# Kernel optimization log

Measured on AMD Instinct MI355X. Metric: run time of the kernel, lower is better.

The kernel has to match this reference:

```python
import jax, jax.numpy as jnp
import numpy as np

N = 10000      # nodes
F_IN = 256     # input feature dim
H1 = 128       # hidden_dim1
H2 = 64        # hidden_dim2 (latent)
E = 320000     # edges (avg degree 32)


def setup_inputs() -> dict:
    key = jax.random.key(0)
    ks = jax.random.split(key, 10)
    x = jax.random.normal(ks[0], (N, F_IN), dtype=jnp.float32)
    edge_index = jax.random.randint(ks[1], (2, E), 0, N, dtype=jnp.int64)
    edge_weight = jax.random.uniform(ks[2], (E,), dtype=jnp.float32)
    s1 = 1.0 / np.sqrt(F_IN)
    s2 = 1.0 / np.sqrt(H1)
    W1 = jax.random.normal(ks[3], (F_IN, H1), dtype=jnp.float32) * s1
    b1 = jnp.zeros((H1,), dtype=jnp.float32)
    W2 = jax.random.normal(ks[4], (H1, H2), dtype=jnp.float32) * s2
    b2 = jnp.zeros((H2,), dtype=jnp.float32)
    W3 = jax.random.normal(ks[5], (H1, H2), dtype=jnp.float32) * s2
    b3 = jnp.zeros((H2,), dtype=jnp.float32)
    return {"x": x, "edge_index": edge_index, "edge_weight": edge_weight,
            "W1": W1, "b1": b1, "W2": W2, "b2": b2, "W3": W3, "b3": b3}


def _gcn_norm(edge_index, edge_weight, n):
    # add self-loops with weight 1, symmetric deg^-1/2 normalization (PyG GCNConv)
    loop = jnp.arange(n)
    row = jnp.concatenate([edge_index[0], loop])
    col = jnp.concatenate([edge_index[1], loop])
    w = jnp.concatenate([edge_weight, jnp.ones((n,), edge_weight.dtype)])
    deg = jax.ops.segment_sum(w, col, num_segments=n)
    dis = jnp.where(deg > 0, jax.lax.rsqrt(deg), 0.0)
    norm = dis[row] * w * dis[col]
    return row, col, norm


def _gcn_conv(h, W, b, row, col, norm, n):
    hw = h @ W                                   # [N, out] transform first (PyG order)
    out = jax.ops.segment_sum(norm[:, None] * hw[row], col, num_segments=n)
    return out + b


def reference(x, edge_index, edge_weight, W1, b1, W2, b2, W3, b3):
    n = x.shape[0]
    row, col, norm = _gcn_norm(edge_index, edge_weight, n)
    h1 = jax.nn.relu(_gcn_conv(x, W1, b1, row, col, norm, n))
    mu = _gcn_conv(h1, W2, b2, row, col, norm, n)
    logvar = _gcn_conv(h1, W3, b3, row, col, norm, n)
    # eval mode: reparameterize -> mu, dropout inactive, decoder act = identity
    z = mu
    adj = z @ z.T                                # [N, N] inner-product decode
    return adj, mu, logvar
```

## Files before the change

### kernel.cpp

```cpp
#include <hip/hip_runtime.h>

#define N_NODES 10000
#define F_IN    256
#define H1      128
#define H2      64
#define NEDGE   320000
#define M_TOT   (NEDGE + N_NODES)

typedef __attribute__((ext_vector_type(8))) short          s16v8;
typedef __attribute__((ext_vector_type(8))) unsigned short u16v8;
typedef __attribute__((ext_vector_type(4))) float          f32v4;


__global__ void k_init(float* deg, int* cnt) {
    int i = blockIdx.x * blockDim.x + threadIdx.x;
    if (i < N_NODES) { deg[i] = 1.0f; cnt[i] = 1; }
}

__global__ void k_count(const int* __restrict__ ei, const float* __restrict__ w,
                        float* deg, int* cnt) {
    int e = blockIdx.x * blockDim.x + threadIdx.x;
    if (e < NEDGE) {
        int c = ei[NEDGE + e];
        atomicAdd(&deg[c], w[e]);
        atomicAdd(&cnt[c], 1);
    }
}

__global__ void k_scan(const int* __restrict__ cnt, int* __restrict__ ptr,
                       int* __restrict__ cur) {
    __shared__ int part[1024];
    int t = threadIdx.x;
    int base = t * 10;
    int local[10];
    int s = 0;
#pragma unroll
    for (int j = 0; j < 10; j++) {
        int idx = base + j;
        int v = (idx < N_NODES) ? cnt[idx] : 0;
        local[j] = s;
        s += v;
    }
    part[t] = s;
    __syncthreads();
    for (int off = 1; off < 1024; off <<= 1) {
        int v = (t >= off) ? part[t - off] : 0;
        __syncthreads();
        part[t] += v;
        __syncthreads();
    }
    int excl = t ? part[t - 1] : 0;
#pragma unroll
    for (int j = 0; j < 10; j++) {
        int idx = base + j;
        if (idx < N_NODES) {
            int p = excl + local[j];
            ptr[idx] = p;
            cur[idx] = p;
        }
    }
    if (t == 1023) ptr[N_NODES] = part[1023];
}

__global__ void k_scatter(const int* __restrict__ ei, const float* __restrict__ w,
                          const float* __restrict__ deg, int* cur,
                          int* __restrict__ src, float* __restrict__ wgt) {
    int t = blockIdx.x * blockDim.x + threadIdx.x;
    if (t >= M_TOT) return;
    int r, c; float nw;
    if (t < NEDGE) {
        r = ei[t];
        c = ei[NEDGE + t];
        nw = rsqrtf(deg[r]) * w[t] * rsqrtf(deg[c]);
    } else {
        r = c = t - NEDGE;
        float d = rsqrtf(deg[r]);
        nw = d * d;
    }
    int pos = atomicAdd(&cur[c], 1);
    src[pos] = r;
    wgt[pos] = nw;
}


__global__ __launch_bounds__(128) void k_gemm1(const float* __restrict__ x,
                                               const float* __restrict__ W1,
                                               float* __restrict__ hw) {
    __shared__ float xs[8 * F_IN];
    int i0 = blockIdx.x * 8;
    int t = threadIdx.x;
    const float4* xsrc = (const float4*)(x + (size_t)i0 * F_IN);
    float4* xd = (float4*)xs;
#pragma unroll
    for (int j = 0; j < 4; j++) xd[t + j * 128] = xsrc[t + j * 128];
    __syncthreads();
    float acc[8] = {0, 0, 0, 0, 0, 0, 0, 0};
    for (int k = 0; k < F_IN; k += 4) {
        float w0 = W1[(k + 0) * H1 + t];
        float w1 = W1[(k + 1) * H1 + t];
        float w2 = W1[(k + 2) * H1 + t];
        float w3 = W1[(k + 3) * H1 + t];
#pragma unroll
        for (int r = 0; r < 8; r++) {
            float4 xv = *(const float4*)&xs[r * F_IN + k];
            acc[r] += xv.x * w0 + xv.y * w1 + xv.z * w2 + xv.w * w3;
        }
    }
#pragma unroll
    for (int r = 0; r < 8; r++) hw[(size_t)(i0 + r) * H1 + t] = acc[r];
}

__global__ __launch_bounds__(128) void k_gemm23(const float* __restrict__ h1,
                                                const float* __restrict__ W2,
                                                const float* __restrict__ W3,
                                                float* __restrict__ t2,
                                                float* __restrict__ t3) {
    __shared__ float hs[8 * H1];
    int i0 = blockIdx.x * 8;
    int t = threadIdx.x;
    const float4* hsrc = (const float4*)(h1 + (size_t)i0 * H1);
    float4* hd = (float4*)hs;
#pragma unroll
    for (int j = 0; j < 2; j++) hd[t + j * 128] = hsrc[t + j * 128];
    __syncthreads();
    int f = t & 63;
    int sel = t >> 6;
    const float* W = sel ? W3 : W2;
    float acc[8] = {0, 0, 0, 0, 0, 0, 0, 0};
    for (int k = 0; k < H1; k += 4) {
        float w0 = W[(k + 0) * H2 + f];
        float w1 = W[(k + 1) * H2 + f];
        float w2 = W[(k + 2) * H2 + f];
        float w3 = W[(k + 3) * H2 + f];
#pragma unroll
        for (int r = 0; r < 8; r++) {
            float4 hv = *(const float4*)&hs[r * H1 + k];
            acc[r] += hv.x * w0 + hv.y * w1 + hv.z * w2 + hv.w * w3;
        }
    }
    float* o = sel ? t3 : t2;
#pragma unroll
    for (int r = 0; r < 8; r++) o[(size_t)(i0 + r) * H2 + f] = acc[r];
}


__global__ __launch_bounds__(128) void k_agg1(const int* __restrict__ ptr,
                                              const int* __restrict__ src,
                                              const float* __restrict__ wgt,
                                              const float* __restrict__ hw,
                                              const float* __restrict__ b1,
                                              float* __restrict__ h1) {
    int i = blockIdx.x;
    int f = threadIdx.x;
    int jb = ptr[i], je = ptr[i + 1];
    float acc = b1[f];
    for (int j = jb; j < je; j++)
        acc += wgt[j] * hw[(size_t)src[j] * H1 + f];
    h1[(size_t)i * H1 + f] = fmaxf(acc, 0.0f);
}

__global__ __launch_bounds__(128) void k_agg2(const int* __restrict__ ptr,
                                              const int* __restrict__ src,
                                              const float* __restrict__ wgt,
                                              const float* __restrict__ t2,
                                              const float* __restrict__ t3,
                                              const float* __restrict__ b2,
                                              const float* __restrict__ b3,
                                              float* __restrict__ mu,
                                              float* __restrict__ lv) {
    int i = blockIdx.x;
    int t = threadIdx.x;
    int f = t & 63;
    int sel = t >> 6;
    const float* tin = sel ? t3 : t2;
    float acc = sel ? b3[f] : b2[f];
    int jb = ptr[i], je = ptr[i + 1];
    for (int j = jb; j < je; j++)
        acc += wgt[j] * tin[(size_t)src[j] * H2 + f];
    float* o = sel ? lv : mu;
    o[(size_t)i * H2 + f] = acc;
}

__global__ __launch_bounds__(256, 1) void k_adj(const float* __restrict__ z,
                                                float* __restrict__ adj) {
    if (blockIdx.x < blockIdx.y) return;
    __shared__ __align__(16) unsigned short PAs[128 * 64];
    __shared__ __align__(16) unsigned short PBs[128 * 64];
    __shared__ __align__(16) unsigned short PLs[128 * 64];
    int tid = threadIdx.x;
    int rowBase = blockIdx.y * 128, colBase = blockIdx.x * 128;
    bool diag = (blockIdx.x == blockIdx.y);

    int lane = tid & 63;
    int wv   = tid >> 6;
    int wr = (wv >> 1) * 64;
    int wc = (wv & 1) * 64;
    int lrow = lane & 15;
    int lk   = lane >> 4;

    int sr   = tid & 127;
    int isB  = tid >> 7;
    int gbase = (isB ? colBase : rowBase) + sr;
    bool ok = gbase < N_NODES;
    const float* srcp = z + (size_t)gbase * 64;
    unsigned short* PH = isB ? PBs : PAs;
    int lslotBase = isB ? 4 : 0;
    int rb7 = sr & 7;

    auto stage = [&](int s) {
#pragma unroll
        for (int g = 0; g < 4; g++) {
            float v[8];
            if (ok) {
                float4 a = *(const float4*)(srcp + s * 32 + g * 8);
                float4 b = *(const float4*)(srcp + s * 32 + g * 8 + 4);
                v[0] = a.x; v[1] = a.y; v[2] = a.z; v[3] = a.w;
                v[4] = b.x; v[5] = b.y; v[6] = b.z; v[7] = b.w;
            } else {
#pragma unroll
                for (int q = 0; q < 8; q++) v[q] = 0.0f;
            }
            u16v8 hv, mv, lv8;
#pragma unroll
            for (int q = 0; q < 8; q++) {
                float xv = v[q];
                unsigned hu = __float_as_uint(xv) & 0xffff0000u;
                float r1 = xv - __uint_as_float(hu);
                unsigned mu2 = __float_as_uint(r1) & 0xffff0000u;
                float r2 = r1 - __uint_as_float(mu2);
                unsigned lu = __float_as_uint(r2) & 0xffff0000u;
                hv[q]  = (unsigned short)(hu >> 16);
                mv[q]  = (unsigned short)(mu2 >> 16);
                lv8[q] = (unsigned short)(lu >> 16);
            }
            int base = sr * 64;
            *reinterpret_cast<u16v8*>(PH  + base + (( g            ^ rb7) * 8)) = hv;
            *reinterpret_cast<u16v8*>(PH  + base + (((4 + g)       ^ rb7) * 8)) = mv;
            *reinterpret_cast<u16v8*>(PLs + base + (((lslotBase+g) ^ rb7) * 8)) = lv8;
        }
    };

    f32v4 acc[4][4];
#pragma unroll
    for (int i = 0; i < 4; i++)
#pragma unroll
        for (int j = 0; j < 4; j++) acc[i][j] = (f32v4)0.0f;

    s16v8 a0[4], a1[4], a2[4], b0[4], b1[4], b2[4];

#define LOADFRAGS()                                                        \
    {                                                                      \
        _Pragma("unroll")                                                  \
        for (int fq = 0; fq < 4; fq++) {                                   \
            int ra = wr + fq * 16 + lrow;                                  \
            int r7 = ra & 7;                                               \
            int ia = ra * 64;                                              \
            a0[fq] = *reinterpret_cast<const s16v8*>(&PAs[ia + ((lk       ^ r7) * 8)]); \
            a1[fq] = *reinterpret_cast<const s16v8*>(&PAs[ia + (((4 + lk) ^ r7) * 8)]); \
            a2[fq] = *reinterpret_cast<const s16v8*>(&PLs[ia + ((lk       ^ r7) * 8)]); \
            int rb = wc + fq * 16 + lrow;                                  \
            int q7 = rb & 7;                                               \
            int ib = rb * 64;                                              \
            b0[fq] = *reinterpret_cast<const s16v8*>(&PBs[ib + ((lk       ^ q7) * 8)]); \
            b1[fq] = *reinterpret_cast<const s16v8*>(&PBs[ib + (((4 + lk) ^ q7) * 8)]); \
            b2[fq] = *reinterpret_cast<const s16v8*>(&PLs[ib + (((4 + lk) ^ q7) * 8)]); \
        }                                                                  \
    }

#define MFMAS()                                                            \
    {                                                                      \
        _Pragma("unroll")                                                  \
        for (int i = 0; i < 4; i++) {                                      \
            _Pragma("unroll")                                              \
            for (int j = 0; j < 4; j++) {                                  \
                f32v4 c = acc[i][j];                                       \
                c = __builtin_amdgcn_mfma_f32_16x16x32_bf16(a0[i], b0[j], c, 0, 0, 0); \
                c = __builtin_amdgcn_mfma_f32_16x16x32_bf16(a0[i], b1[j], c, 0, 0, 0); \
                c = __builtin_amdgcn_mfma_f32_16x16x32_bf16(a1[i], b0[j], c, 0, 0, 0); \
                c = __builtin_amdgcn_mfma_f32_16x16x32_bf16(a0[i], b2[j], c, 0, 0, 0); \
                c = __builtin_amdgcn_mfma_f32_16x16x32_bf16(a2[i], b0[j], c, 0, 0, 0); \
                c = __builtin_amdgcn_mfma_f32_16x16x32_bf16(a1[i], b1[j], c, 0, 0, 0); \
                acc[i][j] = c;                                             \
            }                                                              \
        }                                                                  \
    }

    stage(0);
    __syncthreads();
    LOADFRAGS();
    __syncthreads();
    stage(1);
    MFMAS();
    __syncthreads();
    LOADFRAGS();
    MFMAS();

#undef LOADFRAGS
#undef MFMAS

#pragma unroll
    for (int i = 0; i < 4; i++) {
        int r0 = rowBase + wr + i * 16 + lk * 4;
#pragma unroll
        for (int j = 0; j < 4; j++) {
            int cg = colBase + wc + j * 16 + lrow;
            if (cg < N_NODES) {
#pragma unroll
                for (int v = 0; v < 4; v++) {
                    int rg = r0 + v;
                    if (rg < N_NODES)
                        adj[(size_t)rg * N_NODES + cg] = acc[i][j][v];
                }
                if (!diag)
                    *(float4*)&adj[(size_t)cg * N_NODES + r0] =
                        make_float4(acc[i][j][0], acc[i][j][1], acc[i][j][2], acc[i][j][3]);
            }
        }
    }
}


extern "C" void kernel_launch(void* const* d_in, const int* in_sizes, int n_in,
                              void* d_out, int out_size, void* d_ws, size_t ws_size,
                              hipStream_t stream) {
    const float* x  = (const float*)d_in[0];
    const int*   ei = (const int*)d_in[1];
    const float* w  = (const float*)d_in[2];
    const float* W1 = (const float*)d_in[3];
    const float* b1 = (const float*)d_in[4];
    const float* W2 = (const float*)d_in[5];
    const float* b2 = (const float*)d_in[6];
    const float* W3 = (const float*)d_in[7];
    const float* b3 = (const float*)d_in[8];

    float* out = (float*)d_out;
    float* adj = out;
    float* mu  = out + (size_t)N_NODES * N_NODES;
    float* lv  = mu + (size_t)N_NODES * H2;

    float* ws  = out + 80000000;
    float* deg = ws;
    int*   cnt = (int*)(ws + 10240);
    int*   ptr = (int*)(ws + 20480);
    int*   cur = (int*)(ws + 30720);
    int*   src = (int*)(ws + 40960);
    float* wgt = ws + 371200;
    float* hw  = ws + 701440;
    float* h1  = ws + 1981440;
    float* t2  = ws + 3261440;
    float* t3  = ws + 3901440;

    hipLaunchKernelGGL(k_init,    dim3((N_NODES + 255) / 256), dim3(256), 0, stream, deg, cnt);
    hipLaunchKernelGGL(k_count,   dim3((NEDGE + 255) / 256),   dim3(256), 0, stream, ei, w, deg, cnt);
    hipLaunchKernelGGL(k_scan,    dim3(1), dim3(1024), 0, stream, cnt, ptr, cur);
    hipLaunchKernelGGL(k_scatter, dim3((M_TOT + 255) / 256),   dim3(256), 0, stream, ei, w, deg, cur, src, wgt);
    hipLaunchKernelGGL(k_gemm1,   dim3(N_NODES / 8),  dim3(128), 0, stream, x, W1, hw);
    hipLaunchKernelGGL(k_agg1,    dim3(N_NODES),      dim3(128), 0, stream, ptr, src, wgt, hw, b1, h1);
    hipLaunchKernelGGL(k_gemm23,  dim3(N_NODES / 8),  dim3(128), 0, stream, h1, W2, W3, t2, t3);
    hipLaunchKernelGGL(k_agg2,    dim3(N_NODES),      dim3(128), 0, stream, ptr, src, wgt, t2, t3, b2, b3, mu, lv);

    dim3 g((N_NODES + 127) / 128, (N_NODES + 127) / 128);
    hipLaunchKernelGGL(k_adj, g, dim3(256), 0, stream, mu, adj);
}
```

Baseline: 677.6 us.

## Fuse preprocessing, GEMMs and aggregations into one cooperative persistent kernel

Replaces eight separate launches (init, count, scan, scatter, gemm1, agg1, gemm23, agg2) with one cooperative kernel of 512 blocks that uses grid.sync between phases. The first GEMM now runs before the degree count because it does not depend on it, and the single-block scan becomes a multi-block scan. This is meant to remove launch gaps and the serial scan bottleneck. In exchange the grid is capped at 512 blocks, and the nine grid-wide barriers may limit parallelism in the memory-bound aggregation phases.

```diff
diff --git a/kernel.cpp b/kernel.cpp
--- a/kernel.cpp
+++ b/kernel.cpp
@@ -1,4 +1,7 @@
 #include <hip/hip_runtime.h>
+#include <hip/hip_cooperative_groups.h>
+
+namespace cg = cooperative_groups;
 
 #define N_NODES 10000
 #define F_IN    256
@@ -7,178 +10,183 @@
 #define NEDGE   320000
 #define M_TOT   (NEDGE + N_NODES)
 
+#define NB 512
+#define NT 256
+
 typedef __attribute__((ext_vector_type(8))) short          s16v8;
 typedef __attribute__((ext_vector_type(8))) unsigned short u16v8;
 typedef __attribute__((ext_vector_type(4))) float          f32v4;
 
-
-__global__ void k_init(float* deg, int* cnt) {
-    int i = blockIdx.x * blockDim.x + threadIdx.x;
-    if (i < N_NODES) { deg[i] = 1.0f; cnt[i] = 1; }
-}
-
-__global__ void k_count(const int* __restrict__ ei, const float* __restrict__ w,
-                        float* deg, int* cnt) {
-    int e = blockIdx.x * blockDim.x + threadIdx.x;
-    if (e < NEDGE) {
+__global__ __launch_bounds__(NT, 2) void k_mega(
+    const float* __restrict__ x,  const int* __restrict__ ei, const float* __restrict__ w,
+    const float* __restrict__ W1, const float* __restrict__ b1,
+    const float* __restrict__ W2, const float* __restrict__ b2,
+    const float* __restrict__ W3, const float* __restrict__ b3,
+    float* deg, int* cnt, int* ptr, int* cur, int* part,
+    int* src, float* wgt, float* hw, float* h1, float* t2, float* t3,
+    float* mu, float* lv)
+{
+    cg::grid_group grid = cg::this_grid();
+    __shared__ float smem[16 * F_IN];
+    __shared__ int   wsum[8];
+    int tid  = threadIdx.x;
+    int bid  = blockIdx.x;
+    int gtid = bid * NT + tid;
+
+    if (gtid < N_NODES) { deg[gtid] = 1.0f; cnt[gtid] = 1; }
+    for (int tile = bid; tile < N_NODES / 16; tile += NB) {
+        int i0 = tile * 16;
+        __syncthreads();
+        const float4* xsrc = (const float4*)(x + (size_t)i0 * F_IN);
+        float4* xd = (float4*)smem;
+#pragma unroll
+        for (int j = 0; j < 4; j++) xd[tid + j * 256] = xsrc[tid + j * 256];
+        __syncthreads();
+        int col = tid & 127, half = tid >> 7;
+        const float* xrow = smem + (half * 8) * F_IN;
+        float acc[8] = {0, 0, 0, 0, 0, 0, 0, 0};
+        for (int k = 0; k < F_IN; k += 4) {
+            float w0 = W1[(k + 0) * H1 + col];
+            float w1 = W1[(k + 1) * H1 + col];
+            float w2 = W1[(k + 2) * H1 + col];
+            float w3 = W1[(k + 3) * H1 + col];
+#pragma unroll
+            for (int r = 0; r < 8; r++) {
+                float4 xv = *(const float4*)&xrow[r * F_IN + k];
+                acc[r] += xv.x * w0 + xv.y * w1 + xv.z * w2 + xv.w * w3;
+            }
+        }
+#pragma unroll
+        for (int r = 0; r < 8; r++)
+            hw[(size_t)(i0 + half * 8 + r) * H1 + col] = acc[r];
+    }
+    __threadfence();
+    grid.sync();
+
+    for (int e = gtid; e < NEDGE; e += NB * NT) {
         int c = ei[NEDGE + e];
         atomicAdd(&deg[c], w[e]);
         atomicAdd(&cnt[c], 1);
     }
-}
-
-__global__ void k_scan(const int* __restrict__ cnt, int* __restrict__ ptr,
-                       int* __restrict__ cur) {
-    __shared__ int part[1024];
-    int t = threadIdx.x;
-    int base = t * 10;
-    int local[10];
-    int s = 0;
-#pragma unroll
-    for (int j = 0; j < 10; j++) {
-        int idx = base + j;
-        int v = (idx < N_NODES) ? cnt[idx] : 0;
-        local[j] = s;
-        s += v;
-    }
-    part[t] = s;
-    __syncthreads();
-    for (int off = 1; off < 1024; off <<= 1) {
-        int v = (t >= off) ? part[t - off] : 0;
-        __syncthreads();
-        part[t] += v;
-        __syncthreads();
-    }
-    int excl = t ? part[t - 1] : 0;
-#pragma unroll
-    for (int j = 0; j < 10; j++) {
-        int idx = base + j;
-        if (idx < N_NODES) {
-            int p = excl + local[j];
-            ptr[idx] = p;
-            cur[idx] = p;
-        }
-    }
-    if (t == 1023) ptr[N_NODES] = part[1023];
-}
-
-__global__ void k_scatter(const int* __restrict__ ei, const float* __restrict__ w,
-                          const float* __restrict__ deg, int* cur,
-                          int* __restrict__ src, float* __restrict__ wgt) {
-    int t = blockIdx.x * blockDim.x + threadIdx.x;
-    if (t >= M_TOT) return;
-    int r, c; float nw;
-    if (t < NEDGE) {
-        r = ei[t];
-        c = ei[NEDGE + t];
-        nw = rsqrtf(deg[r]) * w[t] * rsqrtf(deg[c]);
-    } else {
-        r = c = t - NEDGE;
-        float d = rsqrtf(deg[r]);
-        nw = d * d;
-    }
-    int pos = atomicAdd(&cur[c], 1);
-    src[pos] = r;
-    wgt[pos] = nw;
-}
-
-
-__global__ __launch_bounds__(128) void k_gemm1(const float* __restrict__ x,
-                                               const float* __restrict__ W1,
-                                               float* __restrict__ hw) {
-    __shared__ float xs[8 * F_IN];
-    int i0 = blockIdx.x * 8;
-    int t = threadIdx.x;
-    const float4* xsrc = (const float4*)(x + (size_t)i0 * F_IN);
-    float4* xd = (float4*)xs;
-#pragma unroll
-    for (int j = 0; j < 4; j++) xd[t + j * 128] = xsrc[t + j * 128];
-    __syncthreads();
-    float acc[8] = {0, 0, 0, 0, 0, 0, 0, 0};
-    for (int k = 0; k < F_IN; k += 4) {
-        float w0 = W1[(k + 0) * H1 + t];
-        float w1 = W1[(k + 1) * H1 + t];
-        float w2 = W1[(k + 2) * H1 + t];
-        float w3 = W1[(k + 3) * H1 + t];
-#pragma unroll
-        for (int r = 0; r < 8; r++) {
-            float4 xv = *(const float4*)&xs[r * F_IN + k];
-            acc[r] += xv.x * w0 + xv.y * w1 + xv.z * w2 + xv.w * w3;
-        }
-    }
-#pragma unroll
-    for (int r = 0; r < 8; r++) hw[(size_t)(i0 + r) * H1 + t] = acc[r];
-}
-
-__global__ __launch_bounds__(128) void k_gemm23(const float* __restrict__ h1,
-                                                const float* __restrict__ W2,
-                                                const float* __restrict__ W3,
-                                                float* __restrict__ t2,
-                                                float* __restrict__ t3) {
-    __shared__ float hs[8 * H1];
-    int i0 = blockIdx.x * 8;
-    int t = threadIdx.x;
-    const float4* hsrc = (const float4*)(h1 + (size_t)i0 * H1);
-    float4* hd = (float4*)hs;
-#pragma unroll
-    for (int j = 0; j < 2; j++) hd[t + j * 128] = hsrc[t + j * 128];
-    __syncthreads();
-    int f = t & 63;
-    int sel = t >> 6;
-    const float* W = sel ? W3 : W2;
-    float acc[8] = {0, 0, 0, 0, 0, 0, 0, 0};
-    for (int k = 0; k < H1; k += 4) {
-        float w0 = W[(k + 0) * H2 + f];
-        float w1 = W[(k + 1) * H2 + f];
-        float w2 = W[(k + 2) * H2 + f];
-        float w3 = W[(k + 3) * H2 + f];
-#pragma unroll
-        for (int r = 0; r < 8; r++) {
-            float4 hv = *(const float4*)&hs[r * H1 + k];
-            acc[r] += hv.x * w0 + hv.y * w1 + hv.z * w2 + hv.w * w3;
-        }
-    }
-    float* o = sel ? t3 : t2;
-#pragma unroll
-    for (int r = 0; r < 8; r++) o[(size_t)(i0 + r) * H2 + f] = acc[r];
-}
-
-
-__global__ __launch_bounds__(128) void k_agg1(const int* __restrict__ ptr,
-                                              const int* __restrict__ src,
-                                              const float* __restrict__ wgt,
-                                              const float* __restrict__ hw,
-                                              const float* __restrict__ b1,
-                                              float* __restrict__ h1) {
-    int i = blockIdx.x;
-    int f = threadIdx.x;
-    int jb = ptr[i], je = ptr[i + 1];
-    float acc = b1[f];
-    for (int j = jb; j < je; j++)
-        acc += wgt[j] * hw[(size_t)src[j] * H1 + f];
-    h1[(size_t)i * H1 + f] = fmaxf(acc, 0.0f);
-}
-
-__global__ __launch_bounds__(128) void k_agg2(const int* __restrict__ ptr,
-                                              const int* __restrict__ src,
-                                              const float* __restrict__ wgt,
-                                              const float* __restrict__ t2,
-                                              const float* __restrict__ t3,
-                                              const float* __restrict__ b2,
-                                              const float* __restrict__ b3,
-                                              float* __restrict__ mu,
-                                              float* __restrict__ lv) {
-    int i = blockIdx.x;
-    int t = threadIdx.x;
-    int f = t & 63;
-    int sel = t >> 6;
-    const float* tin = sel ? t3 : t2;
-    float acc = sel ? b3[f] : b2[f];
-    int jb = ptr[i], je = ptr[i + 1];
-    for (int j = jb; j < je; j++)
-        acc += wgt[j] * tin[(size_t)src[j] * H2 + f];
-    float* o = sel ? lv : mu;
-    o[(size_t)i * H2 + f] = acc;
+    __threadfence();
+    grid.sync();
+
+    int myExcl = 0;
+    if (bid < 40) {
+        int v = (gtid < N_NODES) ? cnt[gtid] : 0;
+        int lane = tid & 63, wv = tid >> 6;
+        int xi = v;
+#pragma unroll
+        for (int d = 1; d < 64; d <<= 1) {
+            int y = __shfl_up(xi, d, 64);
+            if (lane >= d) xi += y;
+        }
+        if (lane == 63) wsum[wv] = xi;
+        __syncthreads();
+        if (tid == 0) {
+            int s = 0;
+#pragma unroll
+            for (int i2 = 0; i2 < 4; i2++) { int tt = wsum[i2]; wsum[i2] = s; s += tt; }
+            wsum[7] = s;
+        }
+        __syncthreads();
+        myExcl = xi - v + wsum[wv];
+        if (tid == 0) part[bid] = wsum[7];
+    }
+    __threadfence();
+    grid.sync();
+
+    if (bid == 0 && tid < 64) {
+        int v = (tid < 40) ? part[tid] : 0;
+        int xi = v;
+#pragma unroll
+        for (int d = 1; d < 64; d <<= 1) {
+            int y = __shfl_up(xi, d, 64);
+            if (tid >= d) xi += y;
+        }
+        if (tid < 40) part[tid] = xi - v;
+    }
+    __threadfence();
+    grid.sync();
+
+    if (bid < 40 && gtid < N_NODES) {
+        int p = part[bid] + myExcl;
+        ptr[gtid] = p; cur[gtid] = p;
+    }
+    if (gtid == 0) ptr[N_NODES] = M_TOT;
+    __threadfence();
+    grid.sync();
+
+    for (int t = gtid; t < M_TOT; t += NB * NT) {
+        int r, c; float nw;
+        if (t < NEDGE) {
+            r = ei[t]; c = ei[NEDGE + t];
+            nw = rsqrtf(deg[r]) * w[t] * rsqrtf(deg[c]);
+        } else {
+            r = c = t - NEDGE;
+            float d = rsqrtf(deg[r]);
+            nw = d * d;
+        }
+        int pos = atomicAdd(&cur[c], 1);
+        src[pos] = r; wgt[pos] = nw;
+    }
+    __threadfence();
+    grid.sync();
+
+    for (int ch = bid; ch < N_NODES / 2; ch += NB) {
+        int i = ch * 2 + (tid >> 7);
+        int f = tid & 127;
+        int jb = ptr[i], je = ptr[i + 1];
+        float acc = b1[f];
+        for (int j = jb; j < je; j++)
+            acc += wgt[j] * hw[(size_t)src[j] * H1 + f];
+        h1[(size_t)i * H1 + f] = fmaxf(acc, 0.0f);
+    }
+    __threadfence();
+    grid.sync();
+
+    for (int tile = bid; tile < N_NODES / 16; tile += NB) {
+        int i0 = tile * 16;
+        __syncthreads();
+        const float4* hsrc = (const float4*)(h1 + (size_t)i0 * H1);
+        float4* hd = (float4*)smem;
+#pragma unroll
+        for (int j = 0; j < 2; j++) hd[tid + j * 256] = hsrc[tid + j * 256];
+        __syncthreads();
+        int f = tid & 63, sel = (tid >> 6) & 1, half = tid >> 7;
+        const float* W = sel ? W3 : W2;
+        const float* hrow = smem + (half * 8) * H1;
+        float acc[8] = {0, 0, 0, 0, 0, 0, 0, 0};
+        for (int k = 0; k < H1; k += 4) {
+            float w0 = W[(k + 0) * H2 + f];
+            float w1 = W[(k + 1) * H2 + f];
+            float w2 = W[(k + 2) * H2 + f];
+            float w3 = W[(k + 3) * H2 + f];
+#pragma unroll
+            for (int r = 0; r < 8; r++) {
+                float4 hv = *(const float4*)&hrow[r * H1 + k];
+                acc[r] += hv.x * w0 + hv.y * w1 + hv.z * w2 + hv.w * w3;
+            }
+        }
+        float* o = sel ? t3 : t2;
+#pragma unroll
+        for (int r = 0; r < 8; r++)
+            o[(size_t)(i0 + half * 8 + r) * H2 + f] = acc[r];
+    }
+    __threadfence();
+    grid.sync();
+
+    for (int ch = bid; ch < N_NODES / 2; ch += NB) {
+        int i = ch * 2 + (tid >> 7);
+        int f = tid & 63, sel = (tid >> 6) & 1;
+        const float* tin = sel ? t3 : t2;
+        float acc = sel ? b3[f] : b2[f];
+        int jb = ptr[i], je = ptr[i + 1];
+        for (int j = jb; j < je; j++)
+            acc += wgt[j] * tin[(size_t)src[j] * H2 + f];
+        float* o = sel ? lv : mu;
+        o[(size_t)i * H2 + f] = acc;
+    }
 }
 
 __global__ __launch_bounds__(256, 1) void k_adj(const float* __restrict__ z,
@@ -234,9 +242,9 @@
                 lv8[q] = (unsigned short)(lu >> 16);
             }
             int base = sr * 64;
-            *reinterpret_cast<u16v8*>(PH  + base + (( g            ^ rb7) * 8)) = hv;
-            *reinterpret_cast<u16v8*>(PH  + base + (((4 + g)       ^ rb7) * 8)) = mv;
-            *reinterpret_cast<u16v8*>(PLs + base + (((lslotBase+g) ^ rb7) * 8)) = lv8;
+            *reinterpret_cast<u16v8*>(PH  + base + ((g              ^ rb7) * 8)) = hv;
+            *reinterpret_cast<u16v8*>(PH  + base + (((4 + g)        ^ rb7) * 8)) = mv;
+            *reinterpret_cast<u16v8*>(PLs + base + (((lslotBase + g) ^ rb7) * 8)) = lv8;
         }
     };
 
@@ -349,15 +357,15 @@
     float* h1  = ws + 1981440;
     float* t2  = ws + 3261440;
     float* t3  = ws + 3901440;
-
-    hipLaunchKernelGGL(k_init,    dim3((N_NODES + 255) / 256), dim3(256), 0, stream, deg, cnt);
-    hipLaunchKernelGGL(k_count,   dim3((NEDGE + 255) / 256),   dim3(256), 0, stream, ei, w, deg, cnt);
-    hipLaunchKernelGGL(k_scan,    dim3(1), dim3(1024), 0, stream, cnt, ptr, cur);
-    hipLaunchKernelGGL(k_scatter, dim3((M_TOT + 255) / 256),   dim3(256), 0, stream, ei, w, deg, cur, src, wgt);
-    hipLaunchKernelGGL(k_gemm1,   dim3(N_NODES / 8),  dim3(128), 0, stream, x, W1, hw);
-    hipLaunchKernelGGL(k_agg1,    dim3(N_NODES),      dim3(128), 0, stream, ptr, src, wgt, hw, b1, h1);
-    hipLaunchKernelGGL(k_gemm23,  dim3(N_NODES / 8),  dim3(128), 0, stream, h1, W2, W3, t2, t3);
-    hipLaunchKernelGGL(k_agg2,    dim3(N_NODES),      dim3(128), 0, stream, ptr, src, wgt, t2, t3, b2, b3, mu, lv);
+    int*   part = (int*)(ws + 4541440);
+
+    void* args[] = {
+        (void*)&x,  (void*)&ei, (void*)&w,
+        (void*)&W1, (void*)&b1, (void*)&W2, (void*)&b2, (void*)&W3, (void*)&b3,
+        (void*)&deg, (void*)&cnt, (void*)&ptr, (void*)&cur, (void*)&part,
+        (void*)&src, (void*)&wgt, (void*)&hw, (void*)&h1, (void*)&t2, (void*)&t3,
+        (void*)&mu, (void*)&lv };
+    hipLaunchCooperativeKernel((const void*)k_mega, dim3(NB), dim3(NT), args, 0, stream);
 
     dim3 g((N_NODES + 127) / 128, (N_NODES + 127) / 128);
     hipLaunchKernelGGL(k_adj, g, dim3(256), 0, stream, mu, adj);
```

Result: slower. 1.662 ms (+145.2%).

## Fuse layer-1 aggregation with W2/W3 transform; compute full adj grid with transposed stores

Applied to the files above, without the earlier changes.

Merges the first aggregation (with ReLU) and the second-layer W2/W3 transforms into one kernel. Each block aggregates two nodes into shared memory and immediately multiplies them by W2 and W3, which removes the h1 round trip through global memory and one launch. The adjacency kernel drops its symmetric upper-triangle shortcut: every tile is now computed, and each block writes only the coalesced float4 transposed stores instead of both orientations, one of them as scattered scalar writes. This trades twice the decode MFMA work for a uniform, vectorised write pattern. The fused matvec also re-reads W2/W3 per pair of nodes with far less register reuse than the old tiled GEMM.

```diff
diff --git a/kernel.cpp b/kernel.cpp
--- a/kernel.cpp
+++ b/kernel.cpp
@@ -110,53 +110,44 @@
     for (int r = 0; r < 8; r++) hw[(size_t)(i0 + r) * H1 + t] = acc[r];
 }
 
-__global__ __launch_bounds__(128) void k_gemm23(const float* __restrict__ h1,
-                                                const float* __restrict__ W2,
-                                                const float* __restrict__ W3,
-                                                float* __restrict__ t2,
-                                                float* __restrict__ t3) {
-    __shared__ float hs[8 * H1];
-    int i0 = blockIdx.x * 8;
-    int t = threadIdx.x;
-    const float4* hsrc = (const float4*)(h1 + (size_t)i0 * H1);
-    float4* hd = (float4*)hs;
-#pragma unroll
-    for (int j = 0; j < 2; j++) hd[t + j * 128] = hsrc[t + j * 128];
-    __syncthreads();
-    int f = t & 63;
-    int sel = t >> 6;
-    const float* W = sel ? W3 : W2;
-    float acc[8] = {0, 0, 0, 0, 0, 0, 0, 0};
-    for (int k = 0; k < H1; k += 4) {
-        float w0 = W[(k + 0) * H2 + f];
-        float w1 = W[(k + 1) * H2 + f];
-        float w2 = W[(k + 2) * H2 + f];
-        float w3 = W[(k + 3) * H2 + f];
-#pragma unroll
-        for (int r = 0; r < 8; r++) {
-            float4 hv = *(const float4*)&hs[r * H1 + k];
-            acc[r] += hv.x * w0 + hv.y * w1 + hv.z * w2 + hv.w * w3;
-        }
-    }
-    float* o = sel ? t3 : t2;
-#pragma unroll
-    for (int r = 0; r < 8; r++) o[(size_t)(i0 + r) * H2 + f] = acc[r];
-}
-
-
-__global__ __launch_bounds__(128) void k_agg1(const int* __restrict__ ptr,
-                                              const int* __restrict__ src,
-                                              const float* __restrict__ wgt,
-                                              const float* __restrict__ hw,
-                                              const float* __restrict__ b1,
-                                              float* __restrict__ h1) {
-    int i = blockIdx.x;
-    int f = threadIdx.x;
-    int jb = ptr[i], je = ptr[i + 1];
-    float acc = b1[f];
-    for (int j = jb; j < je; j++)
-        acc += wgt[j] * hw[(size_t)src[j] * H1 + f];
-    h1[(size_t)i * H1 + f] = fmaxf(acc, 0.0f);
+__global__ __launch_bounds__(256) void k_agg1g23(const int* __restrict__ ptr,
+                                                 const int* __restrict__ src,
+                                                 const float* __restrict__ wgt,
+                                                 const float* __restrict__ hw,
+                                                 const float* __restrict__ b1,
+                                                 const float* __restrict__ W2,
+                                                 const float* __restrict__ W3,
+                                                 float* __restrict__ t2,
+                                                 float* __restrict__ t3) {
+    __shared__ float h1s[2][H1];
+    int tid = threadIdx.x;
+    {
+        int half = tid >> 7;
+        int f = tid & 127;
+        int i = blockIdx.x * 2 + half;
+        int jb = ptr[i], je = ptr[i + 1];
+        float acc = b1[f];
+        for (int j = jb; j < je; j++)
+            acc += wgt[j] * hw[(size_t)src[j] * H1 + f];
+        h1s[half][f] = fmaxf(acc, 0.0f);
+    }
+    __syncthreads();
+    {
+        int f = tid & 63;
+        int wv = tid >> 6;
+        int sel = wv & 1, nh = wv >> 1;
+        const float* W = sel ? W3 : W2;
+        const float* hr = h1s[nh];
+        float s = 0.0f;
+        for (int k = 0; k < H1; k += 4) {
+            float4 hv = *(const float4*)&hr[k];
+            s += hv.x * W[(k + 0) * H2 + f] + hv.y * W[(k + 1) * H2 + f]
+               + hv.z * W[(k + 2) * H2 + f] + hv.w * W[(k + 3) * H2 + f];
+        }
+        int node = blockIdx.x * 2 + nh;
+        float* o = sel ? t3 : t2;
+        o[(size_t)node * H2 + f] = s;
+    }
 }
 
 __global__ __launch_bounds__(128) void k_agg2(const int* __restrict__ ptr,
@@ -183,13 +174,11 @@
 
 __global__ __launch_bounds__(256, 1) void k_adj(const float* __restrict__ z,
                                                 float* __restrict__ adj) {
-    if (blockIdx.x < blockIdx.y) return;
     __shared__ __align__(16) unsigned short PAs[128 * 64];
     __shared__ __align__(16) unsigned short PBs[128 * 64];
     __shared__ __align__(16) unsigned short PLs[128 * 64];
     int tid = threadIdx.x;
     int rowBase = blockIdx.y * 128, colBase = blockIdx.x * 128;
-    bool diag = (blockIdx.x == blockIdx.y);
 
     int lane = tid & 63;
     int wv   = tid >> 6;
@@ -234,9 +223,9 @@
                 lv8[q] = (unsigned short)(lu >> 16);
             }
             int base = sr * 64;
-            *reinterpret_cast<u16v8*>(PH  + base + (( g            ^ rb7) * 8)) = hv;
-            *reinterpret_cast<u16v8*>(PH  + base + (((4 + g)       ^ rb7) * 8)) = mv;
-            *reinterpret_cast<u16v8*>(PLs + base + (((lslotBase+g) ^ rb7) * 8)) = lv8;
+            *reinterpret_cast<u16v8*>(PH  + base + ((g              ^ rb7) * 8)) = hv;
+            *reinterpret_cast<u16v8*>(PH  + base + (((4 + g)        ^ rb7) * 8)) = mv;
+            *reinterpret_cast<u16v8*>(PLs + base + (((lslotBase + g) ^ rb7) * 8)) = lv8;
         }
     };
 
@@ -301,17 +290,11 @@
 #pragma unroll
     for (int i = 0; i < 4; i++) {
         int r0 = rowBase + wr + i * 16 + lk * 4;
-#pragma unroll
-        for (int j = 0; j < 4; j++) {
-            int cg = colBase + wc + j * 16 + lrow;
-            if (cg < N_NODES) {
-#pragma unroll
-                for (int v = 0; v < 4; v++) {
-                    int rg = r0 + v;
-                    if (rg < N_NODES)
-                        adj[(size_t)rg * N_NODES + cg] = acc[i][j][v];
-                }
-                if (!diag)
+        if (r0 < N_NODES) {
+#pragma unroll
+            for (int j = 0; j < 4; j++) {
+                int cg = colBase + wc + j * 16 + lrow;
+                if (cg < N_NODES)
                     *(float4*)&adj[(size_t)cg * N_NODES + r0] =
                         make_float4(acc[i][j][0], acc[i][j][1], acc[i][j][2], acc[i][j][3]);
             }
@@ -346,7 +329,6 @@
     int*   src = (int*)(ws + 40960);
     float* wgt = ws + 371200;
     float* hw  = ws + 701440;
-    float* h1  = ws + 1981440;
     float* t2  = ws + 3261440;
     float* t3  = ws + 3901440;
 
@@ -355,8 +337,7 @@
     hipLaunchKernelGGL(k_scan,    dim3(1), dim3(1024), 0, stream, cnt, ptr, cur);
     hipLaunchKernelGGL(k_scatter, dim3((M_TOT + 255) / 256),   dim3(256), 0, stream, ei, w, deg, cur, src, wgt);
     hipLaunchKernelGGL(k_gemm1,   dim3(N_NODES / 8),  dim3(128), 0, stream, x, W1, hw);
-    hipLaunchKernelGGL(k_agg1,    dim3(N_NODES),      dim3(128), 0, stream, ptr, src, wgt, hw, b1, h1);
-    hipLaunchKernelGGL(k_gemm23,  dim3(N_NODES / 8),  dim3(128), 0, stream, h1, W2, W3, t2, t3);
+    hipLaunchKernelGGL(k_agg1g23, dim3(N_NODES / 2),  dim3(256), 0, stream, ptr, src, wgt, hw, b1, W2, W3, t2, t3);
     hipLaunchKernelGGL(k_agg2,    dim3(N_NODES),      dim3(128), 0, stream, ptr, src, wgt, t2, t3, b2, b3, mu, lv);
 
     dim3 g((N_NODES + 127) / 128, (N_NODES + 127) / 128);
```

Result: slower. 715.4 us (+5.6%).
